# Kernel optimization log

Measured on AMD Instinct MI355X. Metric: run time of the kernel, lower is better.

The kernel has to match this reference:

```python
import jax, jax.numpy as jnp
import numpy as np


def _component_indices(d, j):
    # Butterfly component at level j has block size k = d >> j.
    k = d >> j
    half = k // 2
    base = np.arange(d // k) * k                       # block starts
    p = (base[:, None] + np.arange(half)[None, :]).reshape(-1)  # [d//2]
    q = p + half
    return p, q


def butterfly_rotation(thetas, d):
    """Compose m = log2(d) butterfly components: R = B(d,d) @ B(d,d/2) @ ... @ B(d,2).
    thetas: [m, d//2] Givens angles per component (block-major order as in torch)."""
    m = thetas.shape[0]
    R = jnp.eye(d, dtype=thetas.dtype)
    for j in range(m):
        p, q = _component_indices(d, j)
        c = jnp.cos(thetas[j])
        s = jnp.sin(thetas[j])
        C = jnp.eye(d, dtype=thetas.dtype)
        C = C.at[p, p].set(c)
        C = C.at[q, q].set(c)
        C = C.at[p, q].set(-s)
        C = C.at[q, p].set(s)
        R = R @ C
    return R


def setup_inputs() -> dict:
    key = jax.random.key(0)
    ks = jax.random.split(key, 8)
    N, D_IN, D_OUT, R = 16384, 4096, 4096, 1024
    M = 10  # log2(R)
    return {
        "x": jax.random.normal(ks[0], (N, D_IN), dtype=jnp.float32),
        "W": jax.random.normal(ks[1], (D_OUT, D_IN), dtype=jnp.float32) * 0.02,
        "bias": jax.random.normal(ks[2], (D_OUT,), dtype=jnp.float32) * 0.02,
        "U": jax.random.normal(ks[3], (D_OUT, R), dtype=jnp.float32) * 0.02,
        "S": jax.random.uniform(ks[4], (R,), dtype=jnp.float32),
        "V": jax.random.normal(ks[5], (R, D_IN), dtype=jnp.float32) * 0.02,
        "thetas_u": jax.random.normal(ks[6], (M, R // 2), dtype=jnp.float32) * 0.1,
        "thetas_v": jax.random.normal(ks[7], (M, R // 2), dtype=jnp.float32) * 0.1,
    }


def reference(x, W, bias, U, S, V, thetas_u, thetas_v):
    r = S.shape[0]
    R_U = butterfly_rotation(thetas_u, r)  # [r, r]
    R_V = butterfly_rotation(thetas_v, r)  # [r, r]
    # base_layer(x)
    base = x @ W.T + bias                  # [N, out]
    # adapter: x @ V^T @ R_V @ diag(S) @ R_U^T @ U^T
    h = (x @ V.T) @ R_V                    # [N, r]
    h = h * S                              # diag(S)
    delta = (h @ R_U.T) @ U.T              # [N, out]
    return base + delta
```

## Files before the change

### kernel.cpp

```cpp
#include <hip/hip_runtime.h>
#include <cstdint>
#include <cstddef>


typedef __bf16 bf16x8 __attribute__((ext_vector_type(8)));
typedef float floatx4 __attribute__((ext_vector_type(4)));
typedef unsigned short ushortx8 __attribute__((ext_vector_type(8)));

__device__ __forceinline__ unsigned short f2bf(float f) {
    unsigned int u = __builtin_bit_cast(unsigned int, f);
    u += 0x7FFFu + ((u >> 16) & 1u);
    return (unsigned short)(u >> 16);
}

__device__ __forceinline__ void gld_lds16(const void* g, void* l) {
    __builtin_amdgcn_global_load_lds(
        (const __attribute__((address_space(1))) void*)g,
        (__attribute__((address_space(3))) void*)l,
        16, 0, 0);
}

__device__ __forceinline__ bf16x8 ldsv(const char* p) {
    return __builtin_bit_cast(bf16x8, *(const ushortx8*)p);
}

#define MFMA_BF16(a, b, c) __builtin_amdgcn_mfma_f32_16x16x32_bf16((a), (b), (c), 0, 0, 0)
#define SCHED0() __builtin_amdgcn_sched_barrier(0)

__global__ __launch_bounds__(256) void butterfly_rows_kernel(
    const float* __restrict__ thetas_v, const float* __restrict__ thetas_u,
    const float* __restrict__ S,
    unsigned short* __restrict__ RVsb, unsigned short* __restrict__ RUb)
{
    const int d = 1024;
    __shared__ float w[1024];
    const int b   = blockIdx.x;
    const int mat = b >> 10;
    const int row = b & 1023;
    const float* th = mat ? thetas_u : thetas_v;
    const int t = threadIdx.x;

    for (int i = t; i < d; i += 256) w[i] = (i == row) ? 1.f : 0.f;
    __syncthreads();

    for (int j = 0; j < 10; ++j) {
        const int sh = 9 - j;
        const int halfm1 = (1 << sh) - 1;
        for (int i = t; i < d / 2; i += 256) {
            const int blk = i >> sh;
            const int off = i & halfm1;
            const int p = (blk << (sh + 1)) + off;
            const int q = p + (halfm1 + 1);
            const float theta = th[j * (d / 2) + i];
            float s, c;
            __sincosf(theta, &s, &c);
            const float wp = w[p], wq = w[q];
            w[p] = c * wp + s * wq;
            w[q] = -s * wp + c * wq;
        }
        __syncthreads();
    }

    if (mat == 0) {
        for (int i = t; i < d; i += 256) RVsb[row * d + i] = f2bf(w[i] * S[i]);
    } else {
        for (int i = t; i < d; i += 256) RUb[row * d + i] = f2bf(w[i]);
    }
}

__global__ __launch_bounds__(256) void cvt_f32_bf16_x8(
    const float* __restrict__ src, unsigned short* __restrict__ dst)
{
    const size_t i = ((size_t)blockIdx.x * 256 + threadIdx.x) * 8;
    float4 a = *(const float4*)(src + i);
    float4 b = *(const float4*)(src + i + 4);
    ushortx8 o;
    o[0] = f2bf(a.x); o[1] = f2bf(a.y); o[2] = f2bf(a.z); o[3] = f2bf(a.w);
    o[4] = f2bf(b.x); o[5] = f2bf(b.y); o[6] = f2bf(b.z); o[7] = f2bf(b.w);
    *(ushortx8*)(dst + i) = o;
}

__global__ __launch_bounds__(256) void transpose_to_bf16(
    const float* __restrict__ src, unsigned short* __restrict__ dst,
    int rows, int cols)
{
    __shared__ float tile[32][33];
    const int tx = threadIdx.x & 31, ty = threadIdx.x >> 5;
    const int c0 = blockIdx.x * 32, r0 = blockIdx.y * 32;
    for (int i = 0; i < 32; i += 8)
        tile[ty + i][tx] = src[(size_t)(r0 + ty + i) * cols + c0 + tx];
    __syncthreads();
    for (int i = 0; i < 32; i += 8)
        dst[(size_t)(c0 + ty + i) * rows + r0 + tx] = f2bf(tile[tx][ty + i]);
}

template <int EPI>
__global__ __launch_bounds__(256) void gemm_nt(
    const unsigned short* __restrict__ A,
    const unsigned short* __restrict__ B,
    float* __restrict__ Cf,
    unsigned short* __restrict__ Cb,
    const float* __restrict__ extra,
    int M, int N, int K)
{
    __shared__ __align__(16) unsigned short As[128 * 32];
    __shared__ __align__(16) unsigned short Bs[128 * 32];

    const int tid  = threadIdx.x;
    const int lane = tid & 63;
    const int wave = tid >> 6;
    const int wm = wave >> 1, wn = wave & 1;

    const int m0 = blockIdx.y * 128;
    const int n0 = blockIdx.x * 128;

    const int srow = wave * 32 + (lane >> 2);
    const int scol = (lane & 3) * 8;

    const unsigned short* gA = A + (size_t)(m0 + srow) * K + scol;
    const unsigned short* gB = B + (size_t)(n0 + srow) * K + scol;
    unsigned short* lA = As + wave * 32 * 32;
    unsigned short* lB = Bs + wave * 32 * 32;

    floatx4 acc[4][4];
#pragma unroll
    for (int i = 0; i < 4; ++i)
#pragma unroll
        for (int j = 0; j < 4; ++j) acc[i][j] = (floatx4)0.f;

    const int ar = lane & 15;
    const int ak = (lane >> 4) * 8;

    for (int kk = 0; kk < K; kk += 32) {
        gld_lds16(gA + kk, lA);
        gld_lds16(gA + kk + (size_t)16 * K, lA + 512);
        gld_lds16(gB + kk, lB);
        gld_lds16(gB + kk + (size_t)16 * K, lB + 512);
        __syncthreads();

        bf16x8 af[4], bfr[4];
#pragma unroll
        for (int tm = 0; tm < 4; ++tm)
            af[tm] = __builtin_bit_cast(bf16x8,
                *(const ushortx8*)&As[(wm * 64 + tm * 16 + ar) * 32 + ak]);
#pragma unroll
        for (int tn = 0; tn < 4; ++tn)
            bfr[tn] = __builtin_bit_cast(bf16x8,
                *(const ushortx8*)&Bs[(wn * 64 + tn * 16 + ar) * 32 + ak]);
#pragma unroll
        for (int tm = 0; tm < 4; ++tm)
#pragma unroll
            for (int tn = 0; tn < 4; ++tn)
                acc[tm][tn] = MFMA_BF16(af[tm], bfr[tn], acc[tm][tn]);
        __syncthreads();
    }

#pragma unroll
    for (int tm = 0; tm < 4; ++tm) {
#pragma unroll
        for (int tn = 0; tn < 4; ++tn) {
#pragma unroll
            for (int r = 0; r < 4; ++r) {
                const int row = m0 + wm * 64 + tm * 16 + (lane >> 4) * 4 + r;
                const int col = n0 + wn * 64 + tn * 16 + (lane & 15);
                const float v = acc[tm][tn][r];
                if (EPI == 1) {
                    Cf[(size_t)row * N + col] = v + extra[col];
                } else if (EPI == 2) {
                    Cb[(size_t)row * N + col] = f2bf(v);
                } else {
                    Cb[(size_t)row * N + col] = f2bf(v + extra[(size_t)row * N + col]);
                }
            }
        }
    }
}

template <int EPI>
__global__ __launch_bounds__(512, 2) void gemm256(
    const unsigned short* __restrict__ A,
    const unsigned short* __restrict__ B,
    float* __restrict__ Cf,
    unsigned short* __restrict__ Cb,
    const float* __restrict__ extra,
    int M, int N, int K, int swz_on)
{
    __shared__ __align__(16) unsigned short As[2][2][128][64];
    __shared__ __align__(16) unsigned short Bs[2][2][128][64];

    const int tid  = threadIdx.x;
    const int lane = tid & 63;
    const int wave = tid >> 6;
    const int wm = wave >> 2;
    const int wn = wave & 3;

    int bx = blockIdx.x, by = blockIdx.y;
    if (swz_on) {
        const int gx  = gridDim.x;
        const int nwg = gx * gridDim.y;
        const int f   = by * gx + bx;
        const int g   = (f & 7) * (nwg >> 3) + (f >> 3);
        bx = g % gx;
        by = g / gx;
    }
    const int m0 = by * 256;
    const int n0 = bx * 256;

    const int srow  = tid >> 3;
    const int scolb = (tid & 7) << 4;
    const int scol  = (scolb ^ ((srow & 7) << 4)) >> 1;
    const unsigned short* gA = A + (size_t)(m0 + srow) * K + scol;
    const unsigned short* gB = B + (size_t)(n0 + srow) * K + scol;
    char* lA = (char*)As + (wave << 10);
    char* lB = (char*)Bs + (wave << 10);
    const size_t rs64 = (size_t)64 * K;

    auto stA = [&](int src_t, int dbuf, int h) {
        const unsigned short* s = gA + (size_t)h * 2 * rs64 + (size_t)src_t * 64;
        char* l = lA + dbuf * 32768 + h * 16384;
        gld_lds16(s, l);
        gld_lds16(s + rs64, l + 8192);
    };
    auto stB = [&](int src_t, int dbuf, int h) {
        const unsigned short* s = gB + (size_t)h * 2 * rs64 + (size_t)src_t * 64;
        char* l = lB + dbuf * 32768 + h * 16384;
        gld_lds16(s, l);
        gld_lds16(s + rs64, l + 8192);
    };

    const int fr  = lane & 15;
    const int kg  = lane >> 4;
    const int swz = (fr & 7) << 4;
    const int ca0 = (kg << 4) ^ swz;
    const int ca1 = (64 + (kg << 4)) ^ swz;
    const int arb = (wm * 64 + fr) * 128;
    const int brb = (wn * 32 + fr) * 128;

    floatx4 acc[8][4];
#pragma unroll
    for (int i = 0; i < 8; ++i)
#pragma unroll
        for (int j = 0; j < 4; ++j) acc[i][j] = (floatx4)0.f;

    const int nkt = K >> 6;

    bf16x8 afA[4][2], afB[4][2], b0[2][2], b1[2][2];

    stA(0, 0, 0); stB(0, 0, 0); stB(0, 0, 1); stA(0, 0, 1);
    stA(1, 1, 0);
    asm volatile("s_waitcnt vmcnt(6)" ::: "memory");
    SCHED0();
    __builtin_amdgcn_s_barrier();
    SCHED0();
    {
        const char* Ad = (const char*)As;
#pragma unroll
        for (int mf = 0; mf < 4; ++mf) {
            afA[mf][0] = ldsv(Ad + arb + mf * 2048 + ca0);
            afA[mf][1] = ldsv(Ad + arb + mf * 2048 + ca1);
        }
    }
    SCHED0();

    for (int t = 0; t < nkt; ++t) {
        const int cb = t & 1, nb = cb ^ 1;
        const char* Ad  = (const char*)As + cb * 32768;
        const char* Bd  = (const char*)Bs + cb * 32768;
        const char* Ad2 = (const char*)As + nb * 32768;
        const int t1 = (t + 1 < nkt) ? t + 1 : 0;
        const int t2 = (t + 2 < nkt) ? t + 2 : 0;

        stB(t1, nb, 0);
        asm volatile("s_waitcnt vmcnt(6)" ::: "memory");
        SCHED0();
        __builtin_amdgcn_s_barrier();
        SCHED0();
#pragma unroll
        for (int nf = 0; nf < 2; ++nf) {
            b0[nf][0] = ldsv(Bd + brb + nf * 2048 + ca0);
            b0[nf][1] = ldsv(Bd + brb + nf * 2048 + ca1);
        }
        SCHED0();
#pragma unroll
        for (int nf = 0; nf < 2; ++nf) {
            b1[nf][0] = ldsv(Bd + 16384 + brb + nf * 2048 + ca0);
            b1[nf][1] = ldsv(Bd + 16384 + brb + nf * 2048 + ca1);
        }
        SCHED0();
        __builtin_amdgcn_s_setprio(1);
#pragma unroll
        for (int mf = 0; mf < 4; ++mf)
#pragma unroll
            for (int nf = 0; nf < 2; ++nf) {
                acc[mf][nf] = MFMA_BF16(afA[mf][0], b0[nf][0], acc[mf][nf]);
                acc[mf][nf] = MFMA_BF16(afA[mf][1], b0[nf][1], acc[mf][nf]);
            }
        __builtin_amdgcn_s_setprio(0);
        SCHED0();

        stB(t1, nb, 1);
        asm volatile("s_waitcnt vmcnt(6)" ::: "memory");
        SCHED0();
        __builtin_amdgcn_s_barrier();
        SCHED0();
#pragma unroll
        for (int mf = 0; mf < 4; ++mf) {
            afB[mf][0] = ldsv(Ad + 16384 + arb + mf * 2048 + ca0);
            afB[mf][1] = ldsv(Ad + 16384 + arb + mf * 2048 + ca1);
        }
        SCHED0();
        __builtin_amdgcn_s_setprio(1);
#pragma unroll
        for (int mf = 0; mf < 4; ++mf)
#pragma unroll
            for (int nf = 0; nf < 2; ++nf) {
                acc[mf][2 + nf] = MFMA_BF16(afA[mf][0], b1[nf][0], acc[mf][2 + nf]);
                acc[mf][2 + nf] = MFMA_BF16(afA[mf][1], b1[nf][1], acc[mf][2 + nf]);
            }
        __builtin_amdgcn_s_setprio(0);
        SCHED0();

        stA(t1, nb, 1);
        SCHED0();
        __builtin_amdgcn_s_setprio(1);
#pragma unroll
        for (int mf = 0; mf < 4; ++mf)
#pragma unroll
            for (int nf = 0; nf < 2; ++nf) {
                acc[4 + mf][2 + nf] = MFMA_BF16(afB[mf][0], b1[nf][0], acc[4 + mf][2 + nf]);
                acc[4 + mf][2 + nf] = MFMA_BF16(afB[mf][1], b1[nf][1], acc[4 + mf][2 + nf]);
            }
        __builtin_amdgcn_s_setprio(0);
        SCHED0();

        stA(t2, cb, 0);
        asm volatile("s_waitcnt vmcnt(6)" ::: "memory");
        SCHED0();
        __builtin_amdgcn_s_barrier();
        SCHED0();
        if (t + 1 < nkt) {
#pragma unroll
            for (int mf = 0; mf < 4; ++mf) {
                afA[mf][0] = ldsv(Ad2 + arb + mf * 2048 + ca0);
                afA[mf][1] = ldsv(Ad2 + arb + mf * 2048 + ca1);
            }
        }
        SCHED0();
        __builtin_amdgcn_s_setprio(1);
#pragma unroll
        for (int mf = 0; mf < 4; ++mf)
#pragma unroll
            for (int nf = 0; nf < 2; ++nf) {
                acc[4 + mf][nf] = MFMA_BF16(afB[mf][0], b0[nf][0], acc[4 + mf][nf]);
                acc[4 + mf][nf] = MFMA_BF16(afB[mf][1], b0[nf][1], acc[4 + mf][nf]);
            }
        __builtin_amdgcn_s_setprio(0);
        SCHED0();
    }

    const int er4 = (lane >> 4) << 2;
    const int ec  = lane & 15;
#pragma unroll
    for (int Mq = 0; Mq < 2; ++Mq)
#pragma unroll
        for (int mf = 0; mf < 4; ++mf)
#pragma unroll
            for (int Nq = 0; Nq < 2; ++Nq)
#pragma unroll
                for (int nf = 0; nf < 2; ++nf)
#pragma unroll
                    for (int r = 0; r < 4; ++r) {
                        const int row = m0 + Mq * 128 + wm * 64 + mf * 16 + er4 + r;
                        const int col = n0 + Nq * 128 + wn * 32 + nf * 16 + ec;
                        const float v = acc[Mq * 4 + mf][Nq * 2 + nf][r];
                        if (EPI == 1) {
                            Cf[(size_t)row * N + col] = v + extra[col];
                        } else {
                            Cb[(size_t)row * N + col] = f2bf(v + extra[(size_t)row * N + col]);
                        }
                    }
    (void)M;
}

extern "C" void kernel_launch(void* const* d_in, const int* in_sizes, int n_in,
                              void* d_out, int out_size, void* d_ws, size_t ws_size,
                              hipStream_t stream)
{
    const int NB = 16384, DIN = 4096, DOUT = 4096, R = 1024;

    const float* x    = (const float*)d_in[0];
    const float* W    = (const float*)d_in[1];
    const float* bias = (const float*)d_in[2];
    const float* U    = (const float*)d_in[3];
    const float* S    = (const float*)d_in[4];
    const float* V    = (const float*)d_in[5];
    const float* th_u = (const float*)d_in[6];
    const float* th_v = (const float*)d_in[7];
    float* out = (float*)d_out;

    char* ws = (char*)d_ws;
    size_t off = 0;
    auto alloc = [&](size_t bytes) {
        char* p = ws + off;
        off += (bytes + 255) & ~(size_t)255;
        return p;
    };
    unsigned short* Xb   = (unsigned short*)alloc((size_t)NB * DIN * 2);
    unsigned short* Wctb = (unsigned short*)alloc((size_t)DOUT * DIN * 2);
    unsigned short* RVsb = (unsigned short*)alloc((size_t)R * R * 2);
    unsigned short* RUb  = (unsigned short*)alloc((size_t)R * R * 2);
    unsigned short* Tb   = (unsigned short*)alloc((size_t)R * R * 2);
    unsigned short* Ub   = (unsigned short*)alloc((size_t)DOUT * R * 2);
    unsigned short* Gb   = (unsigned short*)alloc((size_t)DOUT * R * 2);
    unsigned short* Vtb  = (unsigned short*)alloc((size_t)DIN * R * 2);
    if (off > ws_size) return;

    butterfly_rows_kernel<<<2048, 256, 0, stream>>>(th_v, th_u, S, RVsb, RUb);

    cvt_f32_bf16_x8<<<(NB * (size_t)DIN) / 2048, 256, 0, stream>>>(x, Xb);
    cvt_f32_bf16_x8<<<((size_t)DOUT * R) / 2048, 256, 0, stream>>>(U, Ub);
    transpose_to_bf16<<<dim3(DIN / 32, R / 32), 256, 0, stream>>>(V, Vtb, R, DIN);

    gemm_nt<2><<<dim3(R / 128, R / 128), 256, 0, stream>>>(
        RVsb, RUb, nullptr, Tb, nullptr, R, R, R);

    gemm_nt<2><<<dim3(R / 128, DOUT / 128), 256, 0, stream>>>(
        Ub, Tb, nullptr, Gb, nullptr, DOUT, R, R);

    gemm256<3><<<dim3(DIN / 256, DOUT / 256), 512, 0, stream>>>(
        Gb, Vtb, nullptr, Wctb, W, DOUT, DIN, R, 0);

    gemm256<1><<<dim3(DOUT / 256, NB / 256), 512, 0, stream>>>(
        Xb, Wctb, out, nullptr, bias, NB, DOUT, DIN, 1);
}
```

Baseline: 1.128 ms.

## Restructure gemm256 main loop to one barrier per k-tile with staggered wave order

Replaces the four-barrier, quarter-staged k-loop (staggered half-tile prefetches, A fragments carried across iterations) with a simpler double-buffered loop. Each iteration now has one barrier, issues all four next-tile global-to-LDS loads up front, and waits with a vmcnt count. Odd and even waves walk the four MFMA quadrants in opposite orders so their LDS reads and MFMA bursts are offset. This aims to cut barrier stalls and LDS bank contention, but the LDS reads are no longer prefetched ahead of the barrier and the global loads are less spread out.

New measurement: 1.233 ms. 9.4% more time.

```diff
diff --git a/kernel.cpp b/kernel.cpp
--- a/kernel.cpp
+++ b/kernel.cpp
@@ -176,6 +176,32 @@
     }
 }
 
+#define RD_AF0() do { _Pragma("unroll") \
+    for (int mf = 0; mf < 4; ++mf) { \
+        af0[mf][0] = ldsv(Ad + arb + mf * 2048 + ca0); \
+        af0[mf][1] = ldsv(Ad + arb + mf * 2048 + ca1); } } while (0)
+#define RD_AF1() do { _Pragma("unroll") \
+    for (int mf = 0; mf < 4; ++mf) { \
+        af1[mf][0] = ldsv(Ad + 16384 + arb + mf * 2048 + ca0); \
+        af1[mf][1] = ldsv(Ad + 16384 + arb + mf * 2048 + ca1); } } while (0)
+#define RD_B0() do { _Pragma("unroll") \
+    for (int nf = 0; nf < 2; ++nf) { \
+        b0[nf][0] = ldsv(Bd + brb + nf * 2048 + ca0); \
+        b0[nf][1] = ldsv(Bd + brb + nf * 2048 + ca1); } } while (0)
+#define RD_B1() do { _Pragma("unroll") \
+    for (int nf = 0; nf < 2; ++nf) { \
+        b1[nf][0] = ldsv(Bd + 16384 + brb + nf * 2048 + ca0); \
+        b1[nf][1] = ldsv(Bd + 16384 + brb + nf * 2048 + ca1); } } while (0)
+#define MMQ(A_, B_, mo, no) do { \
+    __builtin_amdgcn_s_setprio(1); \
+    _Pragma("unroll") \
+    for (int mf = 0; mf < 4; ++mf) \
+        _Pragma("unroll") \
+        for (int nf = 0; nf < 2; ++nf) { \
+            acc[(mo) + mf][(no) + nf] = MFMA_BF16(A_[mf][0], B_[nf][0], acc[(mo) + mf][(no) + nf]); \
+            acc[(mo) + mf][(no) + nf] = MFMA_BF16(A_[mf][1], B_[nf][1], acc[(mo) + mf][(no) + nf]); } \
+    __builtin_amdgcn_s_setprio(0); } while (0)
+
 template <int EPI>
 __global__ __launch_bounds__(512, 2) void gemm256(
     const unsigned short* __restrict__ A,
@@ -244,118 +270,42 @@
 
     const int nkt = K >> 6;
 
-    bf16x8 afA[4][2], afB[4][2], b0[2][2], b1[2][2];
-
     stA(0, 0, 0); stB(0, 0, 0); stB(0, 0, 1); stA(0, 0, 1);
-    stA(1, 1, 0);
-    asm volatile("s_waitcnt vmcnt(6)" ::: "memory");
-    SCHED0();
-    __builtin_amdgcn_s_barrier();
-    SCHED0();
-    {
-        const char* Ad = (const char*)As;
-#pragma unroll
-        for (int mf = 0; mf < 4; ++mf) {
-            afA[mf][0] = ldsv(Ad + arb + mf * 2048 + ca0);
-            afA[mf][1] = ldsv(Ad + arb + mf * 2048 + ca1);
-        }
-    }
-    SCHED0();
 
     for (int t = 0; t < nkt; ++t) {
         const int cb = t & 1, nb = cb ^ 1;
-        const char* Ad  = (const char*)As + cb * 32768;
-        const char* Bd  = (const char*)Bs + cb * 32768;
-        const char* Ad2 = (const char*)As + nb * 32768;
-        const int t1 = (t + 1 < nkt) ? t + 1 : 0;
-        const int t2 = (t + 2 < nkt) ? t + 2 : 0;
-
-        stB(t1, nb, 0);
-        asm volatile("s_waitcnt vmcnt(6)" ::: "memory");
-        SCHED0();
+        const char* Ad = (const char*)As + cb * 32768;
+        const char* Bd = (const char*)Bs + cb * 32768;
+
         __builtin_amdgcn_s_barrier();
-        SCHED0();
-#pragma unroll
-        for (int nf = 0; nf < 2; ++nf) {
-            b0[nf][0] = ldsv(Bd + brb + nf * 2048 + ca0);
-            b0[nf][1] = ldsv(Bd + brb + nf * 2048 + ca1);
+        if (t + 1 < nkt) {
+            stA(t + 1, nb, 0); stB(t + 1, nb, 0);
+            stB(t + 1, nb, 1); stA(t + 1, nb, 1);
+            asm volatile("s_waitcnt vmcnt(8)" ::: "memory");
+        } else {
+            asm volatile("s_waitcnt vmcnt(0)" ::: "memory");
         }
         SCHED0();
-#pragma unroll
-        for (int nf = 0; nf < 2; ++nf) {
-            b1[nf][0] = ldsv(Bd + 16384 + brb + nf * 2048 + ca0);
-            b1[nf][1] = ldsv(Bd + 16384 + brb + nf * 2048 + ca1);
+
+        bf16x8 af0[4][2], af1[4][2], b0[2][2], b1[2][2];
+
+        if ((wave & 1) == 0) {
+            RD_AF0(); RD_B0();
+            MMQ(af0, b0, 0, 0);
+            RD_B1();
+            MMQ(af0, b1, 0, 2);
+            RD_AF1();
+            MMQ(af1, b1, 4, 2);
+            MMQ(af1, b0, 4, 0);
+        } else {
+            RD_AF1(); RD_B1();
+            MMQ(af1, b1, 4, 2);
+            RD_B0();
+            MMQ(af1, b0, 4, 0);
+            RD_AF0();
+            MMQ(af0, b0, 0, 0);
+            MMQ(af0, b1, 0, 2);
         }
-        SCHED0();
-        __builtin_amdgcn_s_setprio(1);
-#pragma unroll
-        for (int mf = 0; mf < 4; ++mf)
-#pragma unroll
-            for (int nf = 0; nf < 2; ++nf) {
-                acc[mf][nf] = MFMA_BF16(afA[mf][0], b0[nf][0], acc[mf][nf]);
-                acc[mf][nf] = MFMA_BF16(afA[mf][1], b0[nf][1], acc[mf][nf]);
-            }
-        __builtin_amdgcn_s_setprio(0);
-        SCHED0();
-
-        stB(t1, nb, 1);
-        asm volatile("s_waitcnt vmcnt(6)" ::: "memory");
-        SCHED0();
-        __builtin_amdgcn_s_barrier();
-        SCHED0();
-#pragma unroll
-        for (int mf = 0; mf < 4; ++mf) {
-            afB[mf][0] = ldsv(Ad + 16384 + arb + mf * 2048 + ca0);
-            afB[mf][1] = ldsv(Ad + 16384 + arb + mf * 2048 + ca1);
-        }
-        SCHED0();
-        __builtin_amdgcn_s_setprio(1);
-#pragma unroll
-        for (int mf = 0; mf < 4; ++mf)
-#pragma unroll
-            for (int nf = 0; nf < 2; ++nf) {
-                acc[mf][2 + nf] = MFMA_BF16(afA[mf][0], b1[nf][0], acc[mf][2 + nf]);
-                acc[mf][2 + nf] = MFMA_BF16(afA[mf][1], b1[nf][1], acc[mf][2 + nf]);
-            }
-        __builtin_amdgcn_s_setprio(0);
-        SCHED0();
-
-        stA(t1, nb, 1);
-        SCHED0();
-        __builtin_amdgcn_s_setprio(1);
-#pragma unroll
-        for (int mf = 0; mf < 4; ++mf)
-#pragma unroll
-            for (int nf = 0; nf < 2; ++nf) {
-                acc[4 + mf][2 + nf] = MFMA_BF16(afB[mf][0], b1[nf][0], acc[4 + mf][2 + nf]);
-                acc[4 + mf][2 + nf] = MFMA_BF16(afB[mf][1], b1[nf][1], acc[4 + mf][2 + nf]);
-            }
-        __builtin_amdgcn_s_setprio(0);
-        SCHED0();
-
-        stA(t2, cb, 0);
-        asm volatile("s_waitcnt vmcnt(6)" ::: "memory");
-        SCHED0();
-        __builtin_amdgcn_s_barrier();
-        SCHED0();
-        if (t + 1 < nkt) {
-#pragma unroll
-            for (int mf = 0; mf < 4; ++mf) {
-                afA[mf][0] = ldsv(Ad2 + arb + mf * 2048 + ca0);
-                afA[mf][1] = ldsv(Ad2 + arb + mf * 2048 + ca1);
-            }
-        }
-        SCHED0();
-        __builtin_amdgcn_s_setprio(1);
-#pragma unroll
-        for (int mf = 0; mf < 4; ++mf)
-#pragma unroll
-            for (int nf = 0; nf < 2; ++nf) {
-                acc[4 + mf][nf] = MFMA_BF16(afB[mf][0], b0[nf][0], acc[4 + mf][nf]);
-                acc[4 + mf][nf] = MFMA_BF16(afB[mf][1], b0[nf][1], acc[4 + mf][nf]);
-            }
-        __builtin_amdgcn_s_setprio(0);
-        SCHED0();
     }
 
     const int er4 = (lane >> 4) << 2;
```
